# Kernel tuning notes

Hardware: AMD Instinct MI355X
Metric: run time of the kernel (lower is better)

## Reference

```python
import jax, jax.numpy as jnp
import numpy as np

D_MODEL = 1024
HEAD_DIM = 128
SEQ_LEN = 4096
BATCH = 4


def setup_inputs() -> dict:
    key = jax.random.key(0)
    kx, kq, kk, kv, ko = jax.random.split(key, 5)
    s = 1.0 / np.sqrt(D_MODEL)
    so = 1.0 / np.sqrt(HEAD_DIM)
    return {
        "x": jax.random.normal(kx, (SEQ_LEN, BATCH, D_MODEL), dtype=jnp.float32),
        "Wq": jax.random.uniform(kq, (HEAD_DIM, D_MODEL), jnp.float32, -s, s),
        "Wk": jax.random.uniform(kk, (HEAD_DIM, D_MODEL), jnp.float32, -s, s),
        "Wv": jax.random.uniform(kv, (HEAD_DIM, D_MODEL), jnp.float32, -s, s),
        "Wo": jax.random.uniform(ko, (D_MODEL, HEAD_DIM), jnp.float32, -so, so),
    }


def reference(x, Wq, Wk, Wv, Wo):
    # x: (S, B, D)
    S = x.shape[0]
    scale = Wq.shape[0] ** (-0.5)  # head_dim ** -0.5
    # Projections (Linear: x @ W.T) -> (B, S, H)
    Q = jnp.einsum('sbd,hd->bsh', x, Wq)
    K = jnp.einsum('sbd,hd->bsh', x, Wk)
    V = jnp.einsum('sbd,hd->bsh', x, Wv)
    scores = jnp.einsum('bqh,bkh->bqk', Q, K) * scale  # (B, S, S)
    causal = jnp.tril(jnp.ones((S, S), dtype=bool))
    scores = jnp.where(causal[None], scores, -jnp.inf)
    attn = jax.nn.softmax(scores, axis=-1)
    attn = jnp.nan_to_num(attn, nan=0.0)
    out = jnp.einsum('bqk,bkh->bqh', attn, V)  # (B, S, H)
    # out_proj then back to (S, B, D)
    return jnp.einsum('bsh,dh->sbd', out, Wo)
```

## Files before the change

### kernel.cpp

```cpp
#include <hip/hip_runtime.h>
#include <hip/hip_bf16.h>

#define S_LEN 4096
#define BATCH 4
#define DMODEL 1024
#define HDIM 128
#define NSLOT 4

typedef __attribute__((ext_vector_type(8))) short short8;
typedef __attribute__((ext_vector_type(4))) short short4v;
typedef __attribute__((ext_vector_type(4))) float float4v;
typedef __attribute__((ext_vector_type(16))) float float16v;
typedef __attribute__((ext_vector_type(4))) int int4v;

#define MASKVAL (-3.0e38f)
#define MINIT   (-1.0e30f)

static __device__ __forceinline__ unsigned short f2bf(float f) {
    __hip_bfloat16 h = __float2bfloat16(f);
    return *reinterpret_cast<unsigned short*>(&h);
}
static __device__ __forceinline__ unsigned short f2h(float f) {
    _Float16 h = (_Float16)f; return *reinterpret_cast<unsigned short*>(&h);
}
static __device__ __forceinline__ float h2f(unsigned short u) {
    _Float16 h = *reinterpret_cast<_Float16*>(&u); return (float)h;
}

__global__ __launch_bounds__(256) void xprep_kernel(
    const float* __restrict__ x, unsigned short* __restrict__ xf)
{
    int n = blockIdx.x * 256 + threadIdx.x;
    int b = n >> 17;
    int rem = n & 131071;
    int sb = rem >> 10;
    int rem2 = rem & 1023;
    int kq = rem2 >> 4;
    int grp = rem2 & 15;
    int lane0 = grp * 4;
    int par = grp >> 3;
    int s0 = lane0 & 31;
    int k = kq * 16 + par * 8;

    short8 hv[4];
#pragma unroll
    for (int r = 0; r < 4; r++) {
        int s = sb * 32 + s0 + r;
        const float* src = &x[((size_t)s * BATCH + b) * DMODEL + k];
        float4 v0 = *reinterpret_cast<const float4*>(src);
        float4 v1 = *reinterpret_cast<const float4*>(src + 4);
        short8 h;
        h[0] = (short)f2bf(v0.x); h[1] = (short)f2bf(v0.y);
        h[2] = (short)f2bf(v0.z); h[3] = (short)f2bf(v0.w);
        h[4] = (short)f2bf(v1.x); h[5] = (short)f2bf(v1.y);
        h[6] = (short)f2bf(v1.z); h[7] = (short)f2bf(v1.w);
        hv[r] = h;
    }
    size_t addr = (((size_t)b * 128 + sb) * 64 + kq) * 512 + (size_t)lane0 * 8;
#pragma unroll
    for (int r = 0; r < 4; r++)
        *reinterpret_cast<short8*>(xf + addr + r * 8) = hv[r];
}

__global__ __launch_bounds__(256) void wprep_kernel(
    const float* __restrict__ Wq, const float* __restrict__ Wk,
    const float* __restrict__ Wv, unsigned short* __restrict__ Wqf,
    unsigned short* __restrict__ Wkf, unsigned short* __restrict__ Wvf)
{
    const int which = blockIdx.y;
    const float* W = (which == 0) ? Wq : (which == 1) ? Wk : Wv;
    unsigned short* Wf = (which == 0) ? Wqf : (which == 1) ? Wkf : Wvf;
    int n = blockIdx.x * 256 + threadIdx.x;
    int d = n >> 7, k8 = n & 127;
    const float* src = &W[(size_t)d * DMODEL + k8 * 8];
    float4 v0 = *reinterpret_cast<const float4*>(src);
    float4 v1 = *reinterpret_cast<const float4*>(src + 4);
    short8 h;
    h[0] = (short)f2bf(v0.x); h[1] = (short)f2bf(v0.y);
    h[2] = (short)f2bf(v0.z); h[3] = (short)f2bf(v0.w);
    h[4] = (short)f2bf(v1.x); h[5] = (short)f2bf(v1.y);
    h[6] = (short)f2bf(v1.z); h[7] = (short)f2bf(v1.w);
    size_t addr = (((size_t)(d >> 5)) * 64 + (k8 >> 1)) * 512
                + (size_t)(((d & 31) + 32 * (k8 & 1)) * 8);
    *reinterpret_cast<short8*>(Wf + addr) = h;
}

__global__ __launch_bounds__(256, 4) void qkv_gemm_kernel(
    const unsigned short* __restrict__ xf, const unsigned short* __restrict__ Wqf,
    const unsigned short* __restrict__ Wkf, const unsigned short* __restrict__ Wvf,
    unsigned short* __restrict__ Qf, unsigned short* __restrict__ Kf,
    unsigned short* __restrict__ Vf)
{
    __shared__ float cacc[2 * 4096];

    const int t = threadIdx.x;
    const int w = t >> 6;
    const int lane = t & 63;
    const int hi = lane >> 5;
    const int tloc = w & 1;
    const int half = w >> 1;
    const int tile = blockIdx.x * 2 + tloc;
    const int which = tile >> 9;
    const int rem = tile & 511;
    const int b = rem >> 7;
    const int sblk = rem & 127;

    const unsigned short* Wf = (which == 0) ? Wqf : (which == 1) ? Wkf : Wvf;
    const unsigned short* xp =
        xf + (((size_t)b * 128 + sblk) * 64 + half * 32) * 512 + lane * 8;
    const unsigned short* wp = Wf + (size_t)half * 32 * 512 + lane * 8;

    float16v acc[4];
#pragma unroll
    for (int i = 0; i < 4; i++)
#pragma unroll
        for (int r = 0; r < 16; r++) acc[i][r] = 0.f;

    if (which != 2) {
#pragma unroll 2
        for (int ks = 0; ks < 32; ks++) {
            short8 xv = *reinterpret_cast<const short8*>(xp + ks * 512);
#pragma unroll
            for (int db = 0; db < 4; db++) {
                short8 wv = *reinterpret_cast<const short8*>(
                    wp + (size_t)(db * 64 + ks) * 512);
                acc[db] = __builtin_amdgcn_mfma_f32_32x32x16_bf16(
                    wv, xv, acc[db], 0, 0, 0);
            }
        }
    } else {
#pragma unroll 2
        for (int ks = 0; ks < 32; ks++) {
            short8 xv = *reinterpret_cast<const short8*>(xp + ks * 512);
#pragma unroll
            for (int hb = 0; hb < 4; hb++) {
                short8 wv = *reinterpret_cast<const short8*>(
                    wp + (size_t)(hb * 64 + ks) * 512);
                acc[hb] = __builtin_amdgcn_mfma_f32_32x32x16_bf16(
                    xv, wv, acc[hb], 0, 0, 0);
            }
        }
    }

    float* my = cacc + tloc * 4096;
    if (half == 1) {
#pragma unroll
        for (int db = 0; db < 4; db++)
#pragma unroll
            for (int rc = 0; rc < 4; rc++) {
                float4v v;
#pragma unroll
                for (int j = 0; j < 4; j++) v[j] = acc[db][rc * 4 + j];
                *reinterpret_cast<float4v*>(
                    my + (db * 4 + rc) * 256 + lane * 4) = v;
            }
    }
    __syncthreads();
    if (half != 0) return;

#pragma unroll
    for (int db = 0; db < 4; db++)
#pragma unroll
        for (int rc = 0; rc < 4; rc++) {
            float4v v = *reinterpret_cast<const float4v*>(
                my + (db * 4 + rc) * 256 + lane * 4);
#pragma unroll
            for (int j = 0; j < 4; j++) acc[db][rc * 4 + j] += v[j];
        }

    if (which != 2) {
        unsigned short* Of = (which == 0) ? Qf : Kf;
        const float scale = (which == 0) ? 0.08838834764831845f : 1.0f;
#pragma unroll
        for (int db = 0; db < 4; db++)
#pragma unroll
            for (int g = 0; g < 4; g++) {
                int f = db * 2 + (g >> 1);
                size_t addr = (((size_t)b * 128 + sblk) * 8 + f) * 512
                            + (size_t)(((lane & 31) + 32 * (g & 1)) * 8 + 4 * hi);
                short4v ov;
#pragma unroll
                for (int j = 0; j < 4; j++)
                    ov[j] = (short)f2bf(acc[db][g * 4 + j] * scale);
                *reinterpret_cast<short4v*>(Of + addr) = ov;
            }
    } else {
#pragma unroll
        for (int hb = 0; hb < 4; hb++)
#pragma unroll
            for (int g = 0; g < 4; g++) {
                int kt16 = sblk * 2 + (g >> 1);
                size_t addr = (((size_t)b * 256 + kt16) * 4 + hb) * 512
                            + (size_t)(((lane & 31) + 32 * (g & 1)) * 8 + 4 * hi);
                short4v ov;
#pragma unroll
                for (int j = 0; j < 4; j++)
                    ov[j] = (short)f2bf(acc[hb][g * 4 + j]);
                *reinterpret_cast<short4v*>(Vf + addr) = ov;
            }
    }
}

__global__ __launch_bounds__(256) void attn_kernel(
    const unsigned short* __restrict__ Qf, const unsigned short* __restrict__ Kf,
    const unsigned short* __restrict__ Vf, unsigned short* __restrict__ Opart,
    float* __restrict__ Mpart, float* __restrict__ Lpart)
{
    const int t = threadIdx.x;
    const int w = t >> 6;
    const int lane = t & 63;
    const int l31 = lane & 31;
    const int hi = lane >> 5;

    const int i = blockIdx.x;
    const int xx = i & 7, j = i >> 3;
    const int b = xx >> 1;
    const int p = j * 2 + (xx & 1);
    const int qt = 31 - (p & 31);
    const int c = p >> 5;

    const int nkv = 2 * (qt + 1);
    const int csize = (nkv + NSLOT - 1) / NSLOT;
    const int lo = c * csize;
    const int hic = min(lo + csize, nkv);
    if (lo >= hic) return;

    const int qb = qt * 128;
    const int qrow = qb + w * 32 + l31;

    const unsigned short* qp =
        Qf + (((size_t)b * 128 + (qt * 4 + w)) * 8) * 512 + lane * 8;
    short8 qf[8];
#pragma unroll
    for (int f = 0; f < 8; f++)
        qf[f] = *reinterpret_cast<const short8*>(qp + f * 512);

    const unsigned short* kbase =
        Kf + (size_t)b * (S_LEN / 32) * 8 * 512 + lane * 8;
    const unsigned short* vbase =
        Vf + (size_t)b * (S_LEN / 16) * 4 * 512 + lane * 8;

    float m_run = MINIT, l_run = 0.f;
    float16v o[4];
#pragma unroll
    for (int hb = 0; hb < 4; hb++)
#pragma unroll
        for (int r = 0; r < 16; r++) o[hb][r] = 0.f;

    for (int ti = lo; ti < hic; ti++) {
        const int kvb = ti * 64;
        const unsigned short* kp = kbase + (size_t)ti * 8192;

        float16v s0, s1;
#pragma unroll
        for (int r = 0; r < 16; r++) { s0[r] = 0.f; s1[r] = 0.f; }
#pragma unroll
        for (int f = 0; f < 8; f++) {
            short8 k0 = *reinterpret_cast<const short8*>(kp + f * 512);
            short8 k1 = *reinterpret_cast<const short8*>(kp + 4096 + f * 512);
            s0 = __builtin_amdgcn_mfma_f32_32x32x16_bf16(k0, qf[f], s0, 0, 0, 0);
            s1 = __builtin_amdgcn_mfma_f32_32x32x16_bf16(k1, qf[f], s1, 0, 0, 0);
        }

        if (kvb + 63 > qb + w * 32) {
#pragma unroll
            for (int r = 0; r < 16; r++) {
                int kv0 = kvb + (r & 3) + 8 * (r >> 2) + 4 * hi;
                if (kv0 > qrow) s0[r] = MASKVAL;
                if (kv0 + 32 > qrow) s1[r] = MASKVAL;
            }
        }

        float pmax = s0[0];
#pragma unroll
        for (int r = 1; r < 16; r++) pmax = fmaxf(pmax, s0[r]);
#pragma unroll
        for (int r = 0; r < 16; r++) pmax = fmaxf(pmax, s1[r]);
        pmax = fmaxf(pmax, __shfl_xor(pmax, 32));
        float mnew = fmaxf(m_run, pmax);
        float alpha = __expf(m_run - mnew);
        m_run = mnew;
#pragma unroll
        for (int r = 0; r < 16; r++) s0[r] = __expf(s0[r] - mnew);
#pragma unroll
        for (int r = 0; r < 16; r++) s1[r] = __expf(s1[r] - mnew);
        float sum = 0.f;
#pragma unroll
        for (int r = 0; r < 16; r++) sum += s0[r] + s1[r];
        sum += __shfl_xor(sum, 32);
        l_run = l_run * alpha + sum;
#pragma unroll
        for (int hb = 0; hb < 4; hb++) o[hb] = o[hb] * alpha;

        const unsigned short* vp = vbase + (size_t)ti * 8192;
#pragma unroll
        for (int tw = 0; tw < 4; tw++) {
            float pv[8];
#pragma unroll
            for (int jj = 0; jj < 8; jj++)
                pv[jj] = (tw < 2) ? ((tw & 1) ? s0[8 + jj] : s0[jj])
                                  : ((tw & 1) ? s1[8 + jj] : s1[jj]);
            unsigned int A  = (unsigned int)f2bf(pv[0]) | ((unsigned int)f2bf(pv[1]) << 16);
            unsigned int Bw = (unsigned int)f2bf(pv[2]) | ((unsigned int)f2bf(pv[3]) << 16);
            unsigned int C  = (unsigned int)f2bf(pv[4]) | ((unsigned int)f2bf(pv[5]) << 16);
            unsigned int D  = (unsigned int)f2bf(pv[6]) | ((unsigned int)f2bf(pv[7]) << 16);
            unsigned int y1 = (unsigned int)__shfl_xor((int)(hi ? A : C), 32);
            unsigned int y2 = (unsigned int)__shfl_xor((int)(hi ? Bw : D), 32);
            int4v pw;
            pw[0] = (int)(hi ? y1 : A);
            pw[1] = (int)(hi ? y2 : Bw);
            pw[2] = (int)(hi ? C : y1);
            pw[3] = (int)(hi ? D : y2);
            union { int4v iv; short8 s; } pu; pu.iv = pw;
#pragma unroll
            for (int hb = 0; hb < 4; hb++) {
                short8 vf = *reinterpret_cast<const short8*>(
                    vp + (tw * 4 + hb) * 512);
                o[hb] = __builtin_amdgcn_mfma_f32_32x32x16_bf16(vf, pu.s, o[hb], 0, 0, 0);
            }
        }
    }

    const size_t R0 = (size_t)(c * BATCH + b) * S_LEN;
    const float inv = (l_run > 0.f) ? 1.f / l_run : 0.f;
#pragma unroll
    for (int hb = 0; hb < 4; hb++)
#pragma unroll
        for (int g = 0; g < 4; g++) {
            int h0 = hb * 32 + g * 8 + hi * 4;
            short4v ov;
#pragma unroll
            for (int jj = 0; jj < 4; jj++)
                ov[jj] = (short)f2h(o[hb][g * 4 + jj] * inv);
            *reinterpret_cast<short4v*>(&Opart[(R0 + qrow) * HDIM + h0]) = ov;
        }
    if (hi == 0) { Mpart[R0 + qrow] = m_run; Lpart[R0 + qrow] = l_run; }
}

__global__ __launch_bounds__(256) void combine_kernel(
    const unsigned short* __restrict__ Opart, const float* __restrict__ Mpart,
    const float* __restrict__ Lpart, unsigned short* __restrict__ Ob)
{
    const int BS = BATCH * S_LEN;
    int idx = blockIdx.x * 256 + threadIdx.x;
    int r = idx >> 4, hc = (idx & 15) * 8;
    int q = r & (S_LEN - 1);
    int qt = q >> 7;
    int nkv = 2 * (qt + 1);
    int csize = (nkv + NSLOT - 1) / NSLOT;
    int cnt = (nkv + csize - 1) / csize;

    float m = -INFINITY;
    for (int j = 0; j < cnt; j++) m = fmaxf(m, Mpart[j * BS + r]);
    float wsum = 0.f;
    float acc[8];
#pragma unroll
    for (int e = 0; e < 8; e++) acc[e] = 0.f;
    for (int j = 0; j < cnt; j++) {
        float wj = __expf(Mpart[j * BS + r] - m) * Lpart[j * BS + r];
        wsum += wj;
        short8 o = *reinterpret_cast<const short8*>(
            &Opart[((size_t)j * BS + r) * HDIM + hc]);
#pragma unroll
        for (int e = 0; e < 8; e++) acc[e] += wj * h2f((unsigned short)o[e]);
    }
    float inv = 1.f / wsum;
    short8 ob;
#pragma unroll
    for (int e = 0; e < 8; e++) ob[e] = (short)f2bf(acc[e] * inv);
    *reinterpret_cast<short8*>(&Ob[(size_t)r * HDIM + hc]) = ob;
}

__global__ __launch_bounds__(256) void out_proj_kernel(
    const unsigned short* __restrict__ Ob, const float* __restrict__ Wo,
    float* __restrict__ out)
{
    __shared__ unsigned short As[128 * 128];
    __shared__ unsigned short Bs[128 * 128];

    const int t = threadIdx.x;
    const int lane = t & 63, w = t >> 6;
    const int l15 = lane & 15, l4 = lane >> 4;
    const int wr = (w >> 1) * 64, wc = (w & 1) * 64;
    const int s0 = blockIdx.x * 128;
    const int d0 = blockIdx.y * 128;
    const int b = blockIdx.z;

#pragma unroll
    for (int p = 0; p < 8; p++) {
        int e = p * 2048 + t * 8;
        int r = e >> 7, h = e & 127;
        short8 v = *reinterpret_cast<const short8*>(
            &Ob[((size_t)b * S_LEN + s0 + r) * HDIM + h]);
        int off = (r * 256 + h * 2) ^ ((r & 7) << 4);
        *reinterpret_cast<short8*>(reinterpret_cast<char*>(As) + off) = v;
    }
#pragma unroll
    for (int p = 0; p < 16; p++) {
        int e = p * 1024 + t * 4;
        int r = e >> 7, h = e & 127;
        float4 v = *reinterpret_cast<const float4*>(&Wo[(size_t)(d0 + r) * HDIM + h]);
        short4v hh;
        hh[0] = (short)f2bf(v.x); hh[1] = (short)f2bf(v.y);
        hh[2] = (short)f2bf(v.z); hh[3] = (short)f2bf(v.w);
        int off = (r * 256 + h * 2) ^ ((r & 7) << 4);
        *reinterpret_cast<short4v*>(reinterpret_cast<char*>(Bs) + off) = hh;
    }
    __syncthreads();

    float4v acc[4][4];
#pragma unroll
    for (int i = 0; i < 4; i++)
#pragma unroll
        for (int j = 0; j < 4; j++) acc[i][j] = (float4v){0.f, 0.f, 0.f, 0.f};

#pragma unroll
    for (int kk = 0; kk < 4; kk++) {
        short8 a[4], bf[4];
#pragma unroll
        for (int mi = 0; mi < 4; mi++) {
            int row = wr + mi * 16 + l15;
            int off = (row * 256 + (kk * 32 + l4 * 8) * 2) ^ ((row & 7) << 4);
            a[mi] = *reinterpret_cast<const short8*>(
                reinterpret_cast<const char*>(As) + off);
        }
#pragma unroll
        for (int ni = 0; ni < 4; ni++) {
            int row = wc + ni * 16 + l15;
            int off = (row * 256 + (kk * 32 + l4 * 8) * 2) ^ ((row & 7) << 4);
            bf[ni] = *reinterpret_cast<const short8*>(
                reinterpret_cast<const char*>(Bs) + off);
        }
#pragma unroll
        for (int mi = 0; mi < 4; mi++)
#pragma unroll
            for (int ni = 0; ni < 4; ni++)
                acc[mi][ni] = __builtin_amdgcn_mfma_f32_16x16x32_bf16(
                    a[mi], bf[ni], acc[mi][ni], 0, 0, 0);
    }

#pragma unroll
    for (int mi = 0; mi < 4; mi++)
#pragma unroll
        for (int ni = 0; ni < 4; ni++)
#pragma unroll
            for (int r = 0; r < 4; r++) {
                int s = s0 + wr + mi * 16 + l4 * 4 + r;
                int d = d0 + wc + ni * 16 + l15;
                out[((size_t)s * BATCH + b) * DMODEL + d] = acc[mi][ni][r];
            }
}

extern "C" void kernel_launch(void* const* d_in, const int* in_sizes, int n_in,
                              void* d_out, int out_size, void* d_ws, size_t ws_size,
                              hipStream_t stream) {
    const float* x  = (const float*)d_in[0];
    const float* Wq = (const float*)d_in[1];
    const float* Wk = (const float*)d_in[2];
    const float* Wv = (const float*)d_in[3];
    const float* Wo = (const float*)d_in[4];
    float* out = (float*)d_out;

    const size_t BS = (size_t)BATCH * S_LEN;
    unsigned short* xf    = (unsigned short*)d_ws;
    unsigned short* Opart = (unsigned short*)d_ws;
    float* Mpart = (float*)((char*)d_ws + (16u << 20));
    float* Lpart = Mpart + NSLOT * BS;
    unsigned short* Wqf = (unsigned short*)((char*)d_ws + (32u << 20));
    unsigned short* Wkf = Wqf + 131072;
    unsigned short* Wvf = Wkf + 131072;
    unsigned short* Qf  = Wvf + 131072;
    unsigned short* Kf  = Qf + 2097152;
    unsigned short* Vf  = Kf + 2097152;
    unsigned short* Ob  = Vf + 2097152;

    xprep_kernel<<<2048, 256, 0, stream>>>(x, xf);
    wprep_kernel<<<dim3(64, 3), 256, 0, stream>>>(Wq, Wk, Wv, Wqf, Wkf, Wvf);
    qkv_gemm_kernel<<<768, 256, 0, stream>>>(xf, Wqf, Wkf, Wvf, Qf, Kf, Vf);
    attn_kernel<<<512, 256, 0, stream>>>(Qf, Kf, Vf, Opart, Mpart, Lpart);
    combine_kernel<<<1024, 256, 0, stream>>>(Opart, Mpart, Lpart, Ob);
    out_proj_kernel<<<dim3(32, 8, BATCH), 256, 0, stream>>>(Ob, Wo, out);
}
```

Baseline: 147.0 us.

## Prefetch QKV GEMM operands one step ahead and skip fully masked KV tiles per wave

The QKV projection loop is software-pipelined: the next k-step's x and W fragments are loaded into registers while MFMAs run on the current ones. The MFMA section is wrapped in s_setprio, and the fixed occupancy hint is dropped from launch_bounds. In attention, each wave now stops at the last 64-wide KV block that overlaps its own 32 query rows, so trailing fully masked tiles are skipped. The workspace offsets for Mpart and Lpart and the W buffers are moved, and the P-packing and load code is pulled into helpers. The prefetch raises register pressure, and with no occupancy hint the compiler may allocate more registers, which can cut the number of resident waves.

```diff
diff --git a/kernel.cpp b/kernel.cpp
--- a/kernel.cpp
+++ b/kernel.cpp
@@ -25,6 +25,24 @@
 }
 static __device__ __forceinline__ float h2f(unsigned short u) {
     _Float16 h = *reinterpret_cast<_Float16*>(&u); return (float)h;
+}
+static __device__ __forceinline__ short8 ldf(const unsigned short* p) {
+    return *reinterpret_cast<const short8*>(p);
+}
+static __device__ __forceinline__ short8 pack_p(const float* pv, int hi) {
+    unsigned int A  = (unsigned int)f2bf(pv[0]) | ((unsigned int)f2bf(pv[1]) << 16);
+    unsigned int Bw = (unsigned int)f2bf(pv[2]) | ((unsigned int)f2bf(pv[3]) << 16);
+    unsigned int C  = (unsigned int)f2bf(pv[4]) | ((unsigned int)f2bf(pv[5]) << 16);
+    unsigned int D  = (unsigned int)f2bf(pv[6]) | ((unsigned int)f2bf(pv[7]) << 16);
+    unsigned int y1 = (unsigned int)__shfl_xor((int)(hi ? A : C), 32);
+    unsigned int y2 = (unsigned int)__shfl_xor((int)(hi ? Bw : D), 32);
+    int4v pw;
+    pw[0] = (int)(hi ? y1 : A);
+    pw[1] = (int)(hi ? y2 : Bw);
+    pw[2] = (int)(hi ? C : y1);
+    pw[3] = (int)(hi ? D : y2);
+    union { int4v iv; short8 s; } pu; pu.iv = pw;
+    return pu.s;
 }
 
 __global__ __launch_bounds__(256) void xprep_kernel(
@@ -85,7 +103,7 @@
     *reinterpret_cast<short8*>(Wf + addr) = h;
 }
 
-__global__ __launch_bounds__(256, 4) void qkv_gemm_kernel(
+__global__ __launch_bounds__(256) void qkv_gemm_kernel(
     const unsigned short* __restrict__ xf, const unsigned short* __restrict__ Wqf,
     const unsigned short* __restrict__ Wkf, const unsigned short* __restrict__ Wvf,
     unsigned short* __restrict__ Qf, unsigned short* __restrict__ Kf,
@@ -116,29 +134,38 @@
 #pragma unroll
         for (int r = 0; r < 16; r++) acc[i][r] = 0.f;
 
-    if (which != 2) {
-#pragma unroll 2
+    {
+        short8 xA = ldf(xp);
+        short8 wA[4];
+#pragma unroll
+        for (int d4 = 0; d4 < 4; d4++) wA[d4] = ldf(wp + (size_t)(d4 * 64) * 512);
         for (int ks = 0; ks < 32; ks++) {
-            short8 xv = *reinterpret_cast<const short8*>(xp + ks * 512);
-#pragma unroll
-            for (int db = 0; db < 4; db++) {
-                short8 wv = *reinterpret_cast<const short8*>(
-                    wp + (size_t)(db * 64 + ks) * 512);
-                acc[db] = __builtin_amdgcn_mfma_f32_32x32x16_bf16(
-                    wv, xv, acc[db], 0, 0, 0);
-            }
-        }
-    } else {
-#pragma unroll 2
-        for (int ks = 0; ks < 32; ks++) {
-            short8 xv = *reinterpret_cast<const short8*>(xp + ks * 512);
-#pragma unroll
-            for (int hb = 0; hb < 4; hb++) {
-                short8 wv = *reinterpret_cast<const short8*>(
-                    wp + (size_t)(hb * 64 + ks) * 512);
-                acc[hb] = __builtin_amdgcn_mfma_f32_32x32x16_bf16(
-                    xv, wv, acc[hb], 0, 0, 0);
-            }
+            short8 xB = xA;
+            short8 wB[4];
+#pragma unroll
+            for (int d4 = 0; d4 < 4; d4++) wB[d4] = wA[d4];
+            if (ks < 31) {
+                xB = ldf(xp + (ks + 1) * 512);
+#pragma unroll
+                for (int d4 = 0; d4 < 4; d4++)
+                    wB[d4] = ldf(wp + (size_t)(d4 * 64 + ks + 1) * 512);
+            }
+            __builtin_amdgcn_s_setprio(1);
+            if (which != 2) {
+#pragma unroll
+                for (int d4 = 0; d4 < 4; d4++)
+                    acc[d4] = __builtin_amdgcn_mfma_f32_32x32x16_bf16(
+                        wA[d4], xA, acc[d4], 0, 0, 0);
+            } else {
+#pragma unroll
+                for (int d4 = 0; d4 < 4; d4++)
+                    acc[d4] = __builtin_amdgcn_mfma_f32_32x32x16_bf16(
+                        xA, wA[d4], acc[d4], 0, 0, 0);
+            }
+            __builtin_amdgcn_s_setprio(0);
+            xA = xB;
+#pragma unroll
+            for (int d4 = 0; d4 < 4; d4++) wA[d4] = wB[d4];
         }
     }
 
@@ -227,13 +254,15 @@
 
     const int qb = qt * 128;
     const int qrow = qb + w * 32 + l31;
+    const int lastblk = (qb + w * 32 + 31) >> 6;
+    const int myhi = min(hic, lastblk + 1);
 
     const unsigned short* qp =
         Qf + (((size_t)b * 128 + (qt * 4 + w)) * 8) * 512 + lane * 8;
     short8 qf[8];
 #pragma unroll
     for (int f = 0; f < 8; f++)
-        qf[f] = *reinterpret_cast<const short8*>(qp + f * 512);
+        qf[f] = ldf(qp + f * 512);
 
     const unsigned short* kbase =
         Kf + (size_t)b * (S_LEN / 32) * 8 * 512 + lane * 8;
@@ -247,7 +276,7 @@
 #pragma unroll
         for (int r = 0; r < 16; r++) o[hb][r] = 0.f;
 
-    for (int ti = lo; ti < hic; ti++) {
+    for (int ti = lo; ti < myhi; ti++) {
         const int kvb = ti * 64;
         const unsigned short* kp = kbase + (size_t)ti * 8192;
 
@@ -256,8 +285,8 @@
         for (int r = 0; r < 16; r++) { s0[r] = 0.f; s1[r] = 0.f; }
 #pragma unroll
         for (int f = 0; f < 8; f++) {
-            short8 k0 = *reinterpret_cast<const short8*>(kp + f * 512);
-            short8 k1 = *reinterpret_cast<const short8*>(kp + 4096 + f * 512);
+            short8 k0 = ldf(kp + f * 512);
+            short8 k1 = ldf(kp + 4096 + f * 512);
             s0 = __builtin_amdgcn_mfma_f32_32x32x16_bf16(k0, qf[f], s0, 0, 0, 0);
             s1 = __builtin_amdgcn_mfma_f32_32x32x16_bf16(k1, qf[f], s1, 0, 0, 0);
         }
@@ -300,23 +329,11 @@
             for (int jj = 0; jj < 8; jj++)
                 pv[jj] = (tw < 2) ? ((tw & 1) ? s0[8 + jj] : s0[jj])
                                   : ((tw & 1) ? s1[8 + jj] : s1[jj]);
-            unsigned int A  = (unsigned int)f2bf(pv[0]) | ((unsigned int)f2bf(pv[1]) << 16);
-            unsigned int Bw = (unsigned int)f2bf(pv[2]) | ((unsigned int)f2bf(pv[3]) << 16);
-            unsigned int C  = (unsigned int)f2bf(pv[4]) | ((unsigned int)f2bf(pv[5]) << 16);
-            unsigned int D  = (unsigned int)f2bf(pv[6]) | ((unsigned int)f2bf(pv[7]) << 16);
-            unsigned int y1 = (unsigned int)__shfl_xor((int)(hi ? A : C), 32);
-            unsigned int y2 = (unsigned int)__shfl_xor((int)(hi ? Bw : D), 32);
-            int4v pw;
-            pw[0] = (int)(hi ? y1 : A);
-            pw[1] = (int)(hi ? y2 : Bw);
-            pw[2] = (int)(hi ? C : y1);
-            pw[3] = (int)(hi ? D : y2);
-            union { int4v iv; short8 s; } pu; pu.iv = pw;
+            short8 pu = pack_p(pv, hi);
 #pragma unroll
             for (int hb = 0; hb < 4; hb++) {
-                short8 vf = *reinterpret_cast<const short8*>(
-                    vp + (tw * 4 + hb) * 512);
-                o[hb] = __builtin_amdgcn_mfma_f32_32x32x16_bf16(vf, pu.s, o[hb], 0, 0, 0);
+                short8 vf = ldf(vp + (tw * 4 + hb) * 512);
+                o[hb] = __builtin_amdgcn_mfma_f32_32x32x16_bf16(vf, pu, o[hb], 0, 0, 0);
             }
         }
     }
@@ -464,9 +481,9 @@
     const size_t BS = (size_t)BATCH * S_LEN;
     unsigned short* xf    = (unsigned short*)d_ws;
     unsigned short* Opart = (unsigned short*)d_ws;
-    float* Mpart = (float*)((char*)d_ws + (16u << 20));
+    float* Mpart = (float*)((char*)d_ws + (32u << 20));
     float* Lpart = Mpart + NSLOT * BS;
-    unsigned short* Wqf = (unsigned short*)((char*)d_ws + (32u << 20));
+    unsigned short* Wqf = (unsigned short*)((char*)d_ws + (33u << 20));
     unsigned short* Wkf = Wqf + 131072;
     unsigned short* Wvf = Wkf + 131072;
     unsigned short* Qf  = Wvf + 131072;
```

After: 133.1 us. 1.1x faster.
